# Kernel tuning notes

Hardware: AMD Instinct MI355X
Metric: run time of the kernel (lower is better)

The kernel has to match this reference:

```python
import jax, jax.numpy as jnp
import numpy as np

B, N, H = 8192, 8, 1024  # batch, DOF, hidden width; state dim = 2*N


def setup_inputs() -> dict:
    key = jax.random.key(0)
    ks = jax.random.split(key, 4)
    s1 = 1.0 / np.sqrt(2 * N)
    s2 = 1.0 / np.sqrt(H)
    return {
        "x": jax.random.normal(ks[0], (B, 2 * N), dtype=jnp.float32),
        "W1": jax.random.normal(ks[1], (2 * N, H), dtype=jnp.float32) * s1,
        "b1": jnp.zeros((H,), dtype=jnp.float32),
        "W2": jax.random.normal(ks[2], (H, H), dtype=jnp.float32) * s2,
        "b2": jnp.zeros((H,), dtype=jnp.float32),
        "W3": jax.random.normal(ks[3], (H, 1), dtype=jnp.float32) * s2,
        "b3": jnp.zeros((1,), dtype=jnp.float32),
    }


def reference(x, W1, b1, W2, b2, W3, b3):
    def lagrangian(q, qd):
        z = jnp.concatenate([q, qd])           # (2N,)
        h = jax.nn.softplus(z @ W1 + b1)
        h = jax.nn.softplus(h @ W2 + b2)
        return (h @ W3 + b3).sum()             # scalar L(q, qd)

    dL_dq_fn = jax.grad(lagrangian, argnums=0)
    dL_dqd_fn = jax.grad(lagrangian, argnums=1)
    # forward-over-reverse Hessian blocks (cheap: only N tangents)
    H_qdqd_fn = jax.jacfwd(dL_dqd_fn, argnums=1)   # d2L/dqd dqd, (N,N)
    H_qddq_fn = jax.jacfwd(dL_dqd_fn, argnums=0)   # d2L/dqd dq,  (N,N)

    def step(xi):
        q, qd = xi[:N], xi[N:]
        dL_dq = dL_dq_fn(q, qd)                      # (N,)
        M = H_qdqd_fn(q, qd)                         # mass-matrix block
        C = H_qddq_fn(q, qd)
        qdd = jnp.linalg.inv(M) @ (dL_dq - C @ qd)   # (N,)
        return jnp.concatenate([qd, qdd])            # (2N,)

    return jax.vmap(step)(x)
```

## Files before the change

kernel.cpp:

```cpp
#include <hip/hip_runtime.h>
#include <math.h>

#define B_ 8192
#define H_ 1024
#define LDP0 136
#define LDT 148

#define A_SEC 145
#define B_SEC 129
#define A_GRN (12*A_SEC)
#define B_GRN (12*B_SEC)
#define AB_SH ((A_GRN + B_GRN)*8)

typedef short bfrag __attribute__((ext_vector_type(8)));
typedef float f4v  __attribute__((ext_vector_type(4)));

union U8 { unsigned short u[8]; uint4 v; };

__device__ __forceinline__ float sigf(float x){ return 1.0f/(1.0f+__expf(-x)); }

__device__ __forceinline__ unsigned int pkhi(unsigned int u1, unsigned int u0){
  return __builtin_amdgcn_perm(u1, u0, 0x07060302u);
}

__global__ void k1_s1(const float* __restrict__ x, const float* __restrict__ W1,
                      const float* __restrict__ b1, float* __restrict__ s1o){
  __shared__ float xs[16];
  int b = blockIdx.x, t = threadIdx.x;
  if(t < 16) xs[t] = x[b*16 + t];
  __syncthreads();
  for(int h = t; h < H_; h += 256){
    float acc = b1[h];
    #pragma unroll
    for(int j=0;j<16;j++) acc = __fmaf_rn(xs[j], W1[j*H_ + h], acc);
    s1o[(size_t)b*H_ + h] = sigf(acc);
  }
}

__global__ __launch_bounds__(256,3) void k2_s2(const float* __restrict__ s1,
                      const float* __restrict__ W2, const float* __restrict__ b2,
                      float* __restrict__ s2o){
  __shared__ __align__(16) float As[32*LDP0];
  __shared__ __align__(16) float Bs[32*LDP0];
  int t = threadIdx.x, tx = t & 15, ty = t >> 4;
  int m0 = blockIdx.x * 128, n0 = blockIdx.y * 128;
  int jj = t & 31, rb4 = (t >> 5) * 4;
  float acc[8][8];
  #pragma unroll
  for(int i=0;i<8;i++){
    #pragma unroll
    for(int k=0;k<8;k++) acc[i][k]=0.f; }

  for(int jt=0; jt<32; jt++){
    int j0 = jt*32;
    __syncthreads();
    #pragma unroll
    for(int g=0; g<4; g++){
      #pragma unroll
      for(int i=0;i<4;i++){
        int r = rb4 + i + 32*g;
        As[jj*LDP0 + r] = -__logf(1.0f - s1[(size_t)(m0+r)*H_ + j0 + jj]);
      }
    }
    { int jB = t >> 3, kb = (t & 7) * 16;
      const float* src = &W2[(size_t)(j0 + jB)*H_ + n0 + kb];
      #pragma unroll
      for(int c=0;c<4;c++) *(float4*)&Bs[jB*LDP0 + kb + 4*c] = *(const float4*)(src + 4*c);
    }
    __syncthreads();
    #pragma unroll 8
    for(int j=0;j<32;j++){
      float4 a0 = *(const float4*)&As[j*LDP0 + 8*ty];
      float4 a1f= *(const float4*)&As[j*LDP0 + 8*ty+4];
      float4 b0 = *(const float4*)&Bs[j*LDP0 + 4*tx];
      float4 b1f= *(const float4*)&Bs[j*LDP0 + 64 + 4*tx];
      float aa[8] = {a0.x,a0.y,a0.z,a0.w,a1f.x,a1f.y,a1f.z,a1f.w};
      float bb[8] = {b0.x,b0.y,b0.z,b0.w,b1f.x,b1f.y,b1f.z,b1f.w};
      #pragma unroll
      for(int i=0;i<8;i++){
        #pragma unroll
        for(int k=0;k<8;k++) acc[i][k] = __fmaf_rn(aa[i], bb[k], acc[i][k]); }
    }
  }
  float4 bb0 = *(const float4*)&b2[n0 + 4*tx];
  float4 bb1 = *(const float4*)&b2[n0 + 64 + 4*tx];
  #pragma unroll
  for(int i=0;i<8;i++){
    size_t r = (size_t)(m0 + 8*ty + i)*H_;
    float4 o0 = make_float4(sigf(acc[i][0]+bb0.x), sigf(acc[i][1]+bb0.y),
                            sigf(acc[i][2]+bb0.z), sigf(acc[i][3]+bb0.w));
    float4 o1 = make_float4(sigf(acc[i][4]+bb1.x), sigf(acc[i][5]+bb1.y),
                            sigf(acc[i][6]+bb1.z), sigf(acc[i][7]+bb1.w));
    *(float4*)&s2o[r + n0 + 4*tx] = o0;
    *(float4*)&s2o[r + n0 + 64 + 4*tx] = o1;
  }
}

__global__ __launch_bounds__(256,3) void k3_u(const float* __restrict__ s2,
                      const float* __restrict__ W2, const float* __restrict__ W3,
                      float* __restrict__ u){
  __shared__ __align__(16) float As[32*LDP0];
  __shared__ __align__(16) float Bs[32*LDP0];
  int t = threadIdx.x, tx = t & 15, ty = t >> 4;
  int m0 = blockIdx.x * 128, n0 = blockIdx.y * 128;
  int jj = t & 31, rb4 = (t >> 5) * 4;
  float acc[8][8];
  #pragma unroll
  for(int i=0;i<8;i++){
    #pragma unroll
    for(int k=0;k<8;k++) acc[i][k]=0.f; }

  for(int kt=0; kt<32; kt++){
    int k0 = kt*32;
    __syncthreads();
    float w3v = W3[k0 + jj];
    #pragma unroll
    for(int g=0; g<4; g++){
      #pragma unroll
      for(int i=0;i<4;i++){
        int r = rb4 + i + 32*g;
        As[jj*LDP0 + r] = w3v * s2[(size_t)(m0+r)*H_ + k0 + jj];
      }
    }
    { int jcol = t >> 1, kb = (t & 1) * 16;
      const float* src = &W2[(size_t)(n0 + jcol)*H_ + k0 + kb];
      #pragma unroll
      for(int c=0;c<16;c++) Bs[(kb+c)*LDP0 + jcol] = src[c];
    }
    __syncthreads();
    #pragma unroll 8
    for(int j=0;j<32;j++){
      float4 a0 = *(const float4*)&As[j*LDP0 + 8*ty];
      float4 a1f= *(const float4*)&As[j*LDP0 + 8*ty+4];
      float4 b0 = *(const float4*)&Bs[j*LDP0 + 4*tx];
      float4 b1f= *(const float4*)&Bs[j*LDP0 + 64 + 4*tx];
      float aa[8] = {a0.x,a0.y,a0.z,a0.w,a1f.x,a1f.y,a1f.z,a1f.w};
      float bb[8] = {b0.x,b0.y,b0.z,b0.w,b1f.x,b1f.y,b1f.z,b1f.w};
      #pragma unroll
      for(int i=0;i<8;i++){
        #pragma unroll
        for(int k=0;k<8;k++) acc[i][k] = __fmaf_rn(aa[i], bb[k], acc[i][k]); }
    }
  }
  #pragma unroll
  for(int i=0;i<8;i++){
    size_t r = (size_t)(m0 + 8*ty + i)*H_;
    *(float4*)&u[r + n0 + 4*tx]      = make_float4(acc[i][0],acc[i][1],acc[i][2],acc[i][3]);
    *(float4*)&u[r + n0 + 64 + 4*tx] = make_float4(acc[i][4],acc[i][5],acc[i][6],acc[i][7]);
  }
}

__global__ void kF(const float* __restrict__ W1, float* __restrict__ F64){
  int e = blockIdx.x*256 + threadIdx.x;
  int j = e >> 6, p = e & 63;
  F64[e] = W1[(8+(p>>3))*H_ + j] * W1[(8+(p&7))*H_ + j];
}

__global__ __launch_bounds__(256) void k5a(const float* __restrict__ s1,
                      const float* __restrict__ u, const float* __restrict__ F64,
                      float* __restrict__ Hz1M){
  __shared__ __align__(16) float As[32*72];
  __shared__ __align__(16) float Bs[32*72];
  int t = threadIdx.x, tx = t & 15, ty = t >> 4;
  int m0 = blockIdx.x * 64;
  int jj = t & 31, rb8 = (t >> 5) * 8;
  float acc[4][4];
  #pragma unroll
  for(int i=0;i<4;i++){
    #pragma unroll
    for(int k=0;k<4;k++) acc[i][k]=0.f; }

  for(int jt=0; jt<32; jt++){
    int j0 = jt*32;
    __syncthreads();
    #pragma unroll
    for(int g=0; g<8; g++){
      int r = rb8 + g;
      float s = s1[(size_t)(m0+r)*H_ + j0 + jj];
      As[jj*72 + r] = s*(1.0f-s)*u[(size_t)(m0+r)*H_ + j0 + jj];
    }
    { int jB = t >> 3, cb = (t & 7) * 8;
      const float* src = &F64[(j0 + jB)*64 + cb];
      *(float4*)&Bs[jB*72 + cb]   = *(const float4*)(src);
      *(float4*)&Bs[jB*72 + cb+4] = *(const float4*)(src+4);
    }
    __syncthreads();
    #pragma unroll 8
    for(int j=0;j<32;j++){
      float4 a4 = *(const float4*)&As[j*72 + 4*ty];
      float4 b4 = *(const float4*)&Bs[j*72 + 4*tx];
      float aa[4] = {a4.x,a4.y,a4.z,a4.w};
      float bb[4] = {b4.x,b4.y,b4.z,b4.w};
      #pragma unroll
      for(int i=0;i<4;i++){
        #pragma unroll
        for(int k=0;k<4;k++) acc[i][k] = __fmaf_rn(aa[i], bb[k], acc[i][k]); }
    }
  }
  #pragma unroll
  for(int i=0;i<4;i++)
    *(float4*)&Hz1M[(size_t)(m0+4*ty+i)*64 + 4*tx] =
      make_float4(acc[i][0],acc[i][1],acc[i][2],acc[i][3]);
}

__global__ void k5b(const float* __restrict__ s1, const float* __restrict__ u,
                    const float* __restrict__ W1, const float* __restrict__ x,
                    float* __restrict__ dq16){
  int wid = threadIdx.x >> 6, lane = threadIdx.x & 63;
  int b = blockIdx.x*4 + wid;
  float qd[8];
  #pragma unroll
  for(int i=0;i<8;i++) qd[i] = x[b*16 + 8 + i];
  float accd[8] = {0,0,0,0,0,0,0,0};
  float accc[8] = {0,0,0,0,0,0,0,0};
  for(int jb=0;jb<16;jb++){
    int j = jb*64 + lane;
    float s1v = s1[(size_t)b*H_+j], uv = u[(size_t)b*H_+j];
    float g1 = s1v*uv;
    float d1 = (1.0f - s1v)*g1;
    float w1q = 0.f;
    #pragma unroll
    for(int i=0;i<8;i++){ float w = W1[i*H_+j];
      accd[i] = __fmaf_rn(g1, w, accd[i]);
      w1q = __fmaf_rn(qd[i], w, w1q); }
    float dw = d1*w1q;
    #pragma unroll
    for(int m=0;m<8;m++) accc[m] = __fmaf_rn(dw, W1[(8+m)*H_+j], accc[m]);
  }
  #pragma unroll
  for(int i=0;i<8;i++){
    #pragma unroll
    for(int off=1; off<64; off<<=1){
      accd[i] += __shfl_xor(accd[i], off, 64);
      accc[i] += __shfl_xor(accc[i], off, 64);
    }
  }
  if(lane==0){
    #pragma unroll
    for(int i=0;i<8;i++){ dq16[b*16+i] = accd[i]; dq16[b*16+8+i] = accc[i]; }
  }
}

__global__ void kW2T(const float* __restrict__ W2, unsigned short* __restrict__ Wh,
                     unsigned short* __restrict__ Wm, unsigned short* __restrict__ Wl){
  __shared__ float tile[32][132];
  int j0 = blockIdx.x * 32, k0 = blockIdx.y * 128;
  int t = threadIdx.x;
  int lr = t >> 3, lc0 = (t & 7) * 16;
  const float* src = &W2[(size_t)(j0+lr)*H_ + k0 + lc0];
  #pragma unroll
  for(int c=0;c<16;c+=4) *(float4*)&tile[lr][lc0+c] = *(const float4*)(src + c);
  __syncthreads();
  int k = t >> 1;
  #pragma unroll
  for(int o2=0;o2<2;o2++){
    int oc = (t&1)*2 + o2;
    U8 uh, um2, ul2;
    #pragma unroll
    for(int e=0;e<8;e++){
      float a = tile[oc*8+e][k];
      unsigned int ua = __float_as_uint(a);
      unsigned int h = ua & 0xFFFF0000u;
      float r1 = __fsub_rn(a, __uint_as_float(h));
      unsigned int m = __float_as_uint(r1) & 0xFFFF0000u;
      float l = __fsub_rn(r1, __uint_as_float(m));
      uh.u[e]  = (unsigned short)(h >> 16);
      um2.u[e] = (unsigned short)(m >> 16);
      ul2.u[e] = (unsigned short)(__float_as_uint(l) >> 16);
    }
    size_t o = (size_t)(k0+k)*H_ + j0 + oc*8;
    *(uint4*)&Wh[o] = uh.v; *(uint4*)&Wm[o] = um2.v; *(uint4*)&Wl[o] = ul2.v;
  }
}

__global__ __launch_bounds__(256,3) void k4_mfma(
    const float* __restrict__ s1, const float* __restrict__ s2,
    const float* __restrict__ x,  const float* __restrict__ W1,
    const unsigned short* __restrict__ W2Th, const unsigned short* __restrict__ W2Tm,
    const unsigned short* __restrict__ W2Tl,
    const float* __restrict__ W3, float* __restrict__ Mpart){
  __shared__ union {
    unsigned short AB[AB_SH];
    float Td[64*LDT];
  } sm;
  __shared__ float qds[16][8];

  int t = threadIdx.x;
  int wv = t >> 6, lane = t & 63;
  int kb = blockIdx.x & 7, sgp = blockIdx.x >> 3;
  int b0 = sgp*16, k0 = kb*128;

  if(t < 128){ int s = t>>3, i = t&7; qds[s][i] = x[(b0+s)*16 + 8+i]; }

  f4v acc[9][2];
  #pragma unroll
  for(int mt=0;mt<9;mt++){
    #pragma unroll
    for(int n2=0;n2<2;n2++){ acc[mt][n2][0]=0.f; acc[mt][n2][1]=0.f; acc[mt][n2][2]=0.f; acc[mt][n2][3]=0.f; }
  }

  int aoct = t & 3, arow = t >> 2;
  int bn = t >> 1;
  int fr_m = lane & 15, fr_q = lane >> 4;
  int pfm   = fr_m ^ ((fr_m & 8) >> 1);
  int aRd   = fr_q*A_SEC + pfm;
  int bRd   = A_GRN + fr_q*B_SEC + (2*wv)*16 + pfm;
  int bPerm = A_GRN + (bn ^ ((bn & 8) >> 1));

  for(int jt=0; jt<32; jt++){
    int j0 = jt*32;
    __syncthreads();
    #pragma unroll
    for(int pass=0; pass<3; pass++){
      int r = pass*64 + arow;
      if(r < 144){
        float4 w0, w1v, sa, sb;
        if(r < 128){
          int s = r>>3, m = r&7;
          const float* wp = &W1[(size_t)(8+m)*H_ + j0 + aoct*8];
          w0 = *(const float4*)wp; w1v = *(const float4*)(wp+4);
          const float* sp = &s1[(size_t)(b0+s)*H_ + j0 + aoct*8];
          sa = *(const float4*)sp; sb = *(const float4*)(sp+4);
        } else {
          int s = r - 128;
          float g0=0,g1=0,g2=0,g3=0,g4=0,g5=0,g6=0,g7=0;
          #pragma unroll
          for(int i=0;i<8;i++){
            float q = qds[s][i];
            const float* wp = &W1[(size_t)i*H_ + j0 + aoct*8];
            float4 a0 = *(const float4*)wp, a1 = *(const float4*)(wp+4);
            g0 = __fmaf_rn(q, a0.x, g0); g1 = __fmaf_rn(q, a0.y, g1);
            g2 = __fmaf_rn(q, a0.z, g2); g3 = __fmaf_rn(q, a0.w, g3);
            g4 = __fmaf_rn(q, a1.x, g4); g5 = __fmaf_rn(q, a1.y, g5);
            g6 = __fmaf_rn(q, a1.z, g6); g7 = __fmaf_rn(q, a1.w, g7);
          }
          w0 = make_float4(g0,g1,g2,g3); w1v = make_float4(g4,g5,g6,g7);
          const float* sp = &s1[(size_t)(b0+s)*H_ + j0 + aoct*8];
          sa = *(const float4*)sp; sb = *(const float4*)(sp+4);
        }
        float av[8];
        av[0]=__fmul_rn(w0.x,sa.x); av[1]=__fmul_rn(w0.y,sa.y);
        av[2]=__fmul_rn(w0.z,sa.z); av[3]=__fmul_rn(w0.w,sa.w);
        av[4]=__fmul_rn(w1v.x,sb.x); av[5]=__fmul_rn(w1v.y,sb.y);
        av[6]=__fmul_rn(w1v.z,sb.z); av[7]=__fmul_rn(w1v.w,sb.w);
        unsigned int uh[8], um[8], ul[8];
        #pragma unroll
        for(int e=0;e<8;e++){
          unsigned int ua = __float_as_uint(av[e]);
          unsigned int h = ua & 0xFFFF0000u;
          float r1 = __fsub_rn(av[e], __uint_as_float(h));
          unsigned int m = __float_as_uint(r1) & 0xFFFF0000u;
          float l = __fsub_rn(r1, __uint_as_float(m));
          uh[e]=h; um[e]=m; ul[e]=__float_as_uint(l);
        }
        int g0i = aoct*A_SEC + (r ^ ((r & 8) >> 1));
        uint4 vh = make_uint4(pkhi(uh[1],uh[0]), pkhi(uh[3],uh[2]), pkhi(uh[5],uh[4]), pkhi(uh[7],uh[6]));
        uint4 vm = make_uint4(pkhi(um[1],um[0]), pkhi(um[3],um[2]), pkhi(um[5],um[4]), pkhi(um[7],um[6]));
        uint4 vl = make_uint4(pkhi(ul[1],ul[0]), pkhi(ul[3],ul[2]), pkhi(ul[5],ul[4]), pkhi(ul[7],ul[6]));
        *(uint4*)&sm.AB[(g0i            )*8] = vh;
        *(uint4*)&sm.AB[(g0i + 4*A_SEC  )*8] = vm;
        *(uint4*)&sm.AB[(g0i + 8*A_SEC  )*8] = vl;
      }
    }
    #pragma unroll
    for(int o2=0;o2<2;o2++){
      int oc = (t&1)*2 + o2;
      size_t gsrc = (size_t)(k0+bn)*H_ + j0 + oc*8;
      int g0i = bPerm + oc*B_SEC;
      *(uint4*)&sm.AB[(g0i            )*8] = *(const uint4*)&W2Th[gsrc];
      *(uint4*)&sm.AB[(g0i + 4*B_SEC  )*8] = *(const uint4*)&W2Tm[gsrc];
      *(uint4*)&sm.AB[(g0i + 8*B_SEC  )*8] = *(const uint4*)&W2Tl[gsrc];
    }
    __syncthreads();
    bfrag bf[2][3];
    #pragma unroll
    for(int n2=0;n2<2;n2++){
      #pragma unroll
      for(int p=0;p<3;p++) bf[n2][p] = *(bfrag*)&sm.AB[(bRd + p*4*B_SEC + n2*16)*8];
    }
    #pragma unroll
    for(int mt=0; mt<9; mt++){
      bfrag a0 = *(bfrag*)&sm.AB[(aRd             + mt*16)*8];
      bfrag a1v= *(bfrag*)&sm.AB[(aRd + 4*A_SEC   + mt*16)*8];
      bfrag a2v= *(bfrag*)&sm.AB[(aRd + 8*A_SEC   + mt*16)*8];
      #pragma unroll
      for(int n2=0;n2<2;n2++){
        f4v c = acc[mt][n2];
        c = __builtin_amdgcn_mfma_f32_16x16x32_bf16(a2v, bf[n2][1], c, 0,0,0);
        c = __builtin_amdgcn_mfma_f32_16x16x32_bf16(a1v, bf[n2][2], c, 0,0,0);
        c = __builtin_amdgcn_mfma_f32_16x16x32_bf16(a2v, bf[n2][0], c, 0,0,0);
        c = __builtin_amdgcn_mfma_f32_16x16x32_bf16(a0,  bf[n2][2], c, 0,0,0);
        c = __builtin_amdgcn_mfma_f32_16x16x32_bf16(a1v, bf[n2][1], c, 0,0,0);
        c = __builtin_amdgcn_mfma_f32_16x16x32_bf16(a1v, bf[n2][0], c, 0,0,0);
        c = __builtin_amdgcn_mfma_f32_16x16x32_bf16(a0,  bf[n2][1], c, 0,0,0);
        c = __builtin_amdgcn_mfma_f32_16x16x32_bf16(a0,  bf[n2][0], c, 0,0,0);
        acc[mt][n2] = c;
      }
    }
  }

  float Mp[44];
  #pragma unroll
  for(int i=0;i<44;i++) Mp[i]=0.f;
  int es = t>>4, ec = t&15;
  const float* s2p = &s2[(size_t)(b0+es)*H_ + k0];

  #pragma unroll
  for(int ph=0; ph<2; ph++){
    __syncthreads();
    if((wv>>1) == ph){
      int w1b = wv & 1;
      #pragma unroll
      for(int mt=0; mt<9; mt++){
        #pragma unroll
        for(int n2=0;n2<2;n2++){
          int col = (2*w1b+n2)*16 + fr_m;
          int rowb = mt*16 + fr_q*4;
          #pragma unroll
          for(int rg=0;rg<4;rg++)
            sm.Td[col*LDT + rowb + rg] = acc[mt][n2][rg];
        }
      }
    }
    __syncthreads();
    float4 s2v = *(const float4*)&s2p[ph*64 + ec*4];
    float4 w3v = *(const float4*)&W3[k0 + ph*64 + ec*4];
    float dv[4] = { w3v.x*s2v.x*(1.f-s2v.x), w3v.y*s2v.y*(1.f-s2v.y),
                    w3v.z*s2v.z*(1.f-s2v.z), w3v.w*s2v.w*(1.f-s2v.w) };
    #pragma unroll
    for(int e=0;e<4;e++){
      int col = ec*4+e;
      const float* tp = &sm.Td[col*LDT + es*8];
      float4 t0 = *(const float4*)tp, t1 = *(const float4*)(tp+4);
      float T8[8] = {t0.x,t0.y,t0.z,t0.w,t1.x,t1.y,t1.z,t1.w};
      float vv = sm.Td[col*LDT + 128 + es];
      float d = dv[e];
      int ix=0;
      #pragma unroll
      for(int m=0;m<8;m++){
        float w = __fmul_rn(T8[m], d);
        Mp[36+m] = __fmaf_rn(w, vv, Mp[36+m]);
        #pragma unroll
        for(int n=m;n<8;n++){ Mp[ix] = __fmaf_rn(w, T8[n], Mp[ix]); ix++; }
      }
    }
  }
  #pragma unroll
  for(int i=0;i<44;i++){
    #pragma unroll
    for(int off=1; off<16; off<<=1) Mp[i] += __shfl_xor(Mp[i], off, 64);
  }
  if(ec==0){
    float* o = &Mpart[((size_t)(b0+es)*8 + kb)*44];
    #pragma unroll
    for(int i=0;i<44;i++) o[i] = Mp[i];
  }
}

__global__ __launch_bounds__(64) void k6(const float* __restrict__ x,
                    const float* __restrict__ Hz1M, const float* __restrict__ Mpart,
                    const float* __restrict__ dq16, float* __restrict__ out){
  __shared__ double A[64][73];
  int t = threadIdx.x;
  int b = blockIdx.x*64 + t;
  double* Ar = A[t];
  float qd[8];
  #pragma unroll
  for(int j=0;j<8;j++) qd[j] = x[b*16 + 8 + j];
  double Ms[44];
  #pragma unroll
  for(int i=0;i<44;i++) Ms[i]=0.0;
  for(int kb=0;kb<8;kb++){
    const float* mp = &Mpart[((size_t)b*8+kb)*44];
    #pragma unroll
    for(int i=0;i<44;i++) Ms[i] += (double)mp[i];
  }
  #pragma unroll
  for(int i=0;i<8;i++){
    #pragma unroll
    for(int j=0;j<8;j++) Ar[i*9+j] = (double)Hz1M[(size_t)b*64 + i*8 + j];
    Ar[i*9+8] = (double)dq16[b*16+i] - (double)dq16[b*16+8+i] - Ms[36+i];
  }
  { int ix=0;
    for(int m=0;m<8;m++)
      for(int n=m;n<8;n++){
        Ar[m*9+n] += Ms[ix];
        if(n>m) Ar[n*9+m] += Ms[ix];
        ix++;
      }
  }
  for(int c=0;c<8;c++){
    int piv = c; double best = fabs(Ar[c*9+c]);
    for(int rr=c+1; rr<8; rr++){ double v = fabs(Ar[rr*9+c]); if(v>best){best=v;piv=rr;} }
    if(piv!=c){
      for(int cc=c; cc<9; cc++){ double tmp=Ar[c*9+cc]; Ar[c*9+cc]=Ar[piv*9+cc]; Ar[piv*9+cc]=tmp; }
    }
    double inv = 1.0/Ar[c*9+c];
    for(int rr=c+1; rr<8; rr++){
      double f = Ar[rr*9+c]*inv;
      for(int cc=c+1; cc<9; cc++) Ar[rr*9+cc] -= f*Ar[c*9+cc];
    }
  }
  double sol[8];
  #pragma unroll
  for(int i=7;i>=0;i--){
    double s = Ar[i*9+8];
    #pragma unroll
    for(int j=i+1;j<8;j++) s -= Ar[i*9+j]*sol[j];
    sol[i] = s/Ar[i*9+i];
  }
  #pragma unroll
  for(int j=0;j<8;j++) out[b*16+j] = qd[j];
  #pragma unroll
  for(int i=0;i<8;i++) out[b*16+8+i] = (float)sol[i];
}

extern "C" void kernel_launch(void* const* d_in, const int* in_sizes, int n_in,
                              void* d_out, int out_size, void* d_ws, size_t ws_size,
                              hipStream_t stream){
  const float* x  = (const float*)d_in[0];
  const float* W1 = (const float*)d_in[1];
  const float* b1 = (const float*)d_in[2];
  const float* W2 = (const float*)d_in[3];
  const float* b2 = (const float*)d_in[4];
  const float* W3 = (const float*)d_in[5];
  float* out = (float*)d_out;

  float* ws   = (float*)d_ws;
  size_t BH   = (size_t)B_*H_;
  float* s1   = ws;
  float* s2   = s1  + BH;
  float* u    = s2  + BH;
  float* F64  = u   + BH;
  float* Hz1M = F64 + (size_t)H_*64;
  float* dq16 = Hz1M+ (size_t)B_*64;

  float* Mpart = u;
  unsigned short* W2Th = (unsigned short*)(u + 3145728);
  unsigned short* W2Tm = W2Th + (size_t)H_*H_;
  unsigned short* W2Tl = W2Tm + (size_t)H_*H_;

  k1_s1 <<<dim3(B_),      dim3(256), 0, stream>>>(x, W1, b1, s1);
  k2_s2 <<<dim3(64,8),    dim3(256), 0, stream>>>(s1, W2, b2, s2);
  k3_u  <<<dim3(64,8),    dim3(256), 0, stream>>>(s2, W2, W3, u);
  kF    <<<dim3(256),     dim3(256), 0, stream>>>(W1, F64);
  k5a   <<<dim3(128),     dim3(256), 0, stream>>>(s1, u, F64, Hz1M);
  k5b   <<<dim3(2048),    dim3(256), 0, stream>>>(s1, u, W1, x, dq16);
  kW2T  <<<dim3(32,8),    dim3(256), 0, stream>>>(W2, W2Th, W2Tm, W2Tl);
  k4_mfma<<<dim3(4096),   dim3(256), 0, stream>>>(s1, s2, x, W1, W2Th, W2Tm, W2Tl, W3, Mpart);
  k6    <<<dim3(128),     dim3(64),  0, stream>>>(x, Hz1M, Mpart, dq16, out);
}
```

Baseline: 2.182 ms.

## Load W2 B-fragments directly from global into registers, drop LDS staging

Each wave now loads its own W2 bf16 hi/mid/lo fragments straight from global memory into registers at the top of each j-tile, and no longer stages them through shared memory. This shrinks the LDS footprint to the A operand only, and the occupancy hint rises from 3 to 4 blocks per CU. It removes the LDS store/load round trip for B. In exchange each wave issues uncoalesced 16-byte global loads per row, and register pressure rises under the tighter launch bound.

```diff
diff --git a/kernel.cpp b/kernel.cpp
--- a/kernel.cpp
+++ b/kernel.cpp
@@ -7,10 +7,7 @@
 #define LDT 148
 
 #define A_SEC 145
-#define B_SEC 129
 #define A_GRN (12*A_SEC)
-#define B_GRN (12*B_SEC)
-#define AB_SH ((A_GRN + B_GRN)*8)
 
 typedef short bfrag __attribute__((ext_vector_type(8)));
 typedef float f4v  __attribute__((ext_vector_type(4)));
@@ -273,14 +270,14 @@
   }
 }
 
-__global__ __launch_bounds__(256,3) void k4_mfma(
+__global__ __launch_bounds__(256,4) void k4_mfma(
     const float* __restrict__ s1, const float* __restrict__ s2,
     const float* __restrict__ x,  const float* __restrict__ W1,
     const unsigned short* __restrict__ W2Th, const unsigned short* __restrict__ W2Tm,
     const unsigned short* __restrict__ W2Tl,
     const float* __restrict__ W3, float* __restrict__ Mpart){
   __shared__ union {
-    unsigned short AB[AB_SH];
+    unsigned short A[A_GRN*8];
     float Td[64*LDT];
   } sm;
   __shared__ float qds[16][8];
@@ -300,15 +297,21 @@
   }
 
   int aoct = t & 3, arow = t >> 2;
-  int bn = t >> 1;
   int fr_m = lane & 15, fr_q = lane >> 4;
   int pfm   = fr_m ^ ((fr_m & 8) >> 1);
   int aRd   = fr_q*A_SEC + pfm;
-  int bRd   = A_GRN + fr_q*B_SEC + (2*wv)*16 + pfm;
-  int bPerm = A_GRN + (bn ^ ((bn & 8) >> 1));
 
   for(int jt=0; jt<32; jt++){
     int j0 = jt*32;
+    bfrag bf[2][3];
+    #pragma unroll
+    for(int n2=0;n2<2;n2++){
+      int n = (2*wv+n2)*16 + fr_m;
+      size_t gb = (size_t)(k0+n)*H_ + j0 + fr_q*8;
+      bf[n2][0] = *(const bfrag*)&W2Th[gb];
+      bf[n2][1] = *(const bfrag*)&W2Tm[gb];
+      bf[n2][2] = *(const bfrag*)&W2Tl[gb];
+    }
     __syncthreads();
     #pragma unroll
     for(int pass=0; pass<3; pass++){
@@ -357,32 +360,17 @@
         uint4 vh = make_uint4(pkhi(uh[1],uh[0]), pkhi(uh[3],uh[2]), pkhi(uh[5],uh[4]), pkhi(uh[7],uh[6]));
         uint4 vm = make_uint4(pkhi(um[1],um[0]), pkhi(um[3],um[2]), pkhi(um[5],um[4]), pkhi(um[7],um[6]));
         uint4 vl = make_uint4(pkhi(ul[1],ul[0]), pkhi(ul[3],ul[2]), pkhi(ul[5],ul[4]), pkhi(ul[7],ul[6]));
-        *(uint4*)&sm.AB[(g0i            )*8] = vh;
-        *(uint4*)&sm.AB[(g0i + 4*A_SEC  )*8] = vm;
-        *(uint4*)&sm.AB[(g0i + 8*A_SEC  )*8] = vl;
-      }
-    }
-    #pragma unroll
-    for(int o2=0;o2<2;o2++){
-      int oc = (t&1)*2 + o2;
-      size_t gsrc = (size_t)(k0+bn)*H_ + j0 + oc*8;
-      int g0i = bPerm + oc*B_SEC;
-      *(uint4*)&sm.AB[(g0i            )*8] = *(const uint4*)&W2Th[gsrc];
-      *(uint4*)&sm.AB[(g0i + 4*B_SEC  )*8] = *(const uint4*)&W2Tm[gsrc];
-      *(uint4*)&sm.AB[(g0i + 8*B_SEC  )*8] = *(const uint4*)&W2Tl[gsrc];
-    }
-    __syncthreads();
-    bfrag bf[2][3];
-    #pragma unroll
-    for(int n2=0;n2<2;n2++){
-      #pragma unroll
-      for(int p=0;p<3;p++) bf[n2][p] = *(bfrag*)&sm.AB[(bRd + p*4*B_SEC + n2*16)*8];
-    }
+        *(uint4*)&sm.A[(g0i            )*8] = vh;
+        *(uint4*)&sm.A[(g0i + 4*A_SEC  )*8] = vm;
+        *(uint4*)&sm.A[(g0i + 8*A_SEC  )*8] = vl;
+      }
+    }
+    __syncthreads();
     #pragma unroll
     for(int mt=0; mt<9; mt++){
-      bfrag a0 = *(bfrag*)&sm.AB[(aRd             + mt*16)*8];
-      bfrag a1v= *(bfrag*)&sm.AB[(aRd + 4*A_SEC   + mt*16)*8];
-      bfrag a2v= *(bfrag*)&sm.AB[(aRd + 8*A_SEC   + mt*16)*8];
+      bfrag a0 = *(bfrag*)&sm.A[(aRd             + mt*16)*8];
+      bfrag a1v= *(bfrag*)&sm.A[(aRd + 4*A_SEC   + mt*16)*8];
+      bfrag a2v= *(bfrag*)&sm.A[(aRd + 8*A_SEC   + mt*16)*8];
       #pragma unroll
       for(int n2=0;n2<2;n2++){
         f4v c = acc[mt][n2];
```

Measured after the change: 3.196 ms. +46.5%, slower.

## Double k4_mfma output tile width to halve A-tile rebuild work

Applied to the files above, without the earlier changes.

Each k4_mfma block now covers 256 output columns of the hidden layer instead of 128, so each wave computes four 16-column MFMA tiles rather than two. The grid shrinks from 4096 to 2048 blocks. The A tile, which is rebuilt per block with three-way bf16 splitting and tangent computation, is now reused across twice as many columns, cutting redundant A-side global loads and conversion work. The cost is twice as many accumulator registers, larger shared memory for the B tile, and occupancy lowered from 3 to 2 blocks per CU. The epilogue runs in four phases and writes the partial results in the same two 128-column chunks as before.

```diff
diff --git a/kernel.cpp b/kernel.cpp
--- a/kernel.cpp
+++ b/kernel.cpp
@@ -7,10 +7,10 @@
 #define LDT 148
 
 #define A_SEC 145
-#define B_SEC 129
+#define B2_SEC 257
 #define A_GRN (12*A_SEC)
-#define B_GRN (12*B_SEC)
-#define AB_SH ((A_GRN + B_GRN)*8)
+#define B2_GRN (12*B2_SEC)
+#define AB2_SH ((A_GRN + B2_GRN)*8)
 
 typedef short bfrag __attribute__((ext_vector_type(8)));
 typedef float f4v  __attribute__((ext_vector_type(4)));
@@ -273,30 +273,30 @@
   }
 }
 
-__global__ __launch_bounds__(256,3) void k4_mfma(
+__global__ __launch_bounds__(256,2) void k4_mfma(
     const float* __restrict__ s1, const float* __restrict__ s2,
     const float* __restrict__ x,  const float* __restrict__ W1,
     const unsigned short* __restrict__ W2Th, const unsigned short* __restrict__ W2Tm,
     const unsigned short* __restrict__ W2Tl,
     const float* __restrict__ W3, float* __restrict__ Mpart){
   __shared__ union {
-    unsigned short AB[AB_SH];
+    unsigned short AB[AB2_SH];
     float Td[64*LDT];
   } sm;
   __shared__ float qds[16][8];
 
   int t = threadIdx.x;
   int wv = t >> 6, lane = t & 63;
-  int kb = blockIdx.x & 7, sgp = blockIdx.x >> 3;
-  int b0 = sgp*16, k0 = kb*128;
+  int kb2 = blockIdx.x & 3, sgp = blockIdx.x >> 2;
+  int b0 = sgp*16, k0 = kb2*256;
 
   if(t < 128){ int s = t>>3, i = t&7; qds[s][i] = x[(b0+s)*16 + 8+i]; }
 
-  f4v acc[9][2];
+  f4v acc[9][4];
   #pragma unroll
   for(int mt=0;mt<9;mt++){
     #pragma unroll
-    for(int n2=0;n2<2;n2++){ acc[mt][n2][0]=0.f; acc[mt][n2][1]=0.f; acc[mt][n2][2]=0.f; acc[mt][n2][3]=0.f; }
+    for(int n2=0;n2<4;n2++){ acc[mt][n2][0]=0.f; acc[mt][n2][1]=0.f; acc[mt][n2][2]=0.f; acc[mt][n2][3]=0.f; }
   }
 
   int aoct = t & 3, arow = t >> 2;
@@ -304,8 +304,10 @@
   int fr_m = lane & 15, fr_q = lane >> 4;
   int pfm   = fr_m ^ ((fr_m & 8) >> 1);
   int aRd   = fr_q*A_SEC + pfm;
-  int bRd   = A_GRN + fr_q*B_SEC + (2*wv)*16 + pfm;
-  int bPerm = A_GRN + (bn ^ ((bn & 8) >> 1));
+  int bRd   = A_GRN + fr_q*B2_SEC + wv*64 + pfm;
+  int bW0   = A_GRN + (bn ^ ((bn & 8) >> 1));
+  int bn2   = bn + 128;
+  int bW1   = A_GRN + (bn2 ^ ((bn2 & 8) >> 1));
 
   for(int jt=0; jt<32; jt++){
     int j0 = jt*32;
@@ -365,18 +367,23 @@
     #pragma unroll
     for(int o2=0;o2<2;o2++){
       int oc = (t&1)*2 + o2;
-      size_t gsrc = (size_t)(k0+bn)*H_ + j0 + oc*8;
-      int g0i = bPerm + oc*B_SEC;
-      *(uint4*)&sm.AB[(g0i            )*8] = *(const uint4*)&W2Th[gsrc];
-      *(uint4*)&sm.AB[(g0i + 4*B_SEC  )*8] = *(const uint4*)&W2Tm[gsrc];
-      *(uint4*)&sm.AB[(g0i + 8*B_SEC  )*8] = *(const uint4*)&W2Tl[gsrc];
-    }
-    __syncthreads();
-    bfrag bf[2][3];
-    #pragma unroll
-    for(int n2=0;n2<2;n2++){
-      #pragma unroll
-      for(int p=0;p<3;p++) bf[n2][p] = *(bfrag*)&sm.AB[(bRd + p*4*B_SEC + n2*16)*8];
+      size_t gs0 = (size_t)(k0+bn )*H_ + j0 + oc*8;
+      size_t gs1 = (size_t)(k0+bn2)*H_ + j0 + oc*8;
+      int w0i = bW0 + oc*B2_SEC;
+      int w1i = bW1 + oc*B2_SEC;
+      *(uint4*)&sm.AB[(w0i             )*8] = *(const uint4*)&W2Th[gs0];
+      *(uint4*)&sm.AB[(w0i + 4*B2_SEC  )*8] = *(const uint4*)&W2Tm[gs0];
+      *(uint4*)&sm.AB[(w0i + 8*B2_SEC  )*8] = *(const uint4*)&W2Tl[gs0];
+      *(uint4*)&sm.AB[(w1i             )*8] = *(const uint4*)&W2Th[gs1];
+      *(uint4*)&sm.AB[(w1i + 4*B2_SEC  )*8] = *(const uint4*)&W2Tm[gs1];
+      *(uint4*)&sm.AB[(w1i + 8*B2_SEC  )*8] = *(const uint4*)&W2Tl[gs1];
+    }
+    __syncthreads();
+    bfrag bf[4][3];
+    #pragma unroll
+    for(int n2=0;n2<4;n2++){
+      #pragma unroll
+      for(int p=0;p<3;p++) bf[n2][p] = *(bfrag*)&sm.AB[(bRd + p*4*B2_SEC + n2*16)*8];
     }
     #pragma unroll
     for(int mt=0; mt<9; mt++){
@@ -384,7 +391,7 @@
       bfrag a1v= *(bfrag*)&sm.AB[(aRd + 4*A_SEC   + mt*16)*8];
       bfrag a2v= *(bfrag*)&sm.AB[(aRd + 8*A_SEC   + mt*16)*8];
       #pragma unroll
-      for(int n2=0;n2<2;n2++){
+      for(int n2=0;n2<4;n2++){
         f4v c = acc[mt][n2];
         c = __builtin_amdgcn_mfma_f32_16x16x32_bf16(a2v, bf[n2][1], c, 0,0,0);
         c = __builtin_amdgcn_mfma_f32_16x16x32_bf16(a1v, bf[n2][2], c, 0,0,0);
@@ -406,15 +413,14 @@
   const float* s2p = &s2[(size_t)(b0+es)*H_ + k0];
 
   #pragma unroll
-  for(int ph=0; ph<2; ph++){
-    __syncthreads();
-    if((wv>>1) == ph){
-      int w1b = wv & 1;
+  for(int ph=0; ph<4; ph++){
+    __syncthreads();
+    if(wv == ph){
       #pragma unroll
       for(int mt=0; mt<9; mt++){
         #pragma unroll
-        for(int n2=0;n2<2;n2++){
-          int col = (2*w1b+n2)*16 + fr_m;
+        for(int n2=0;n2<4;n2++){
+          int col = n2*16 + fr_m;
           int rowb = mt*16 + fr_q*4;
           #pragma unroll
           for(int rg=0;rg<4;rg++)
@@ -444,16 +450,21 @@
         for(int n=m;n<8;n++){ Mp[ix] = __fmaf_rn(w, T8[n], Mp[ix]); ix++; }
       }
     }
-  }
-  #pragma unroll
-  for(int i=0;i<44;i++){
-    #pragma unroll
-    for(int off=1; off<16; off<<=1) Mp[i] += __shfl_xor(Mp[i], off, 64);
-  }
-  if(ec==0){
-    float* o = &Mpart[((size_t)(b0+es)*8 + kb)*44];
-    #pragma unroll
-    for(int i=0;i<44;i++) o[i] = Mp[i];
+    if(ph & 1){
+      #pragma unroll
+      for(int i=0;i<44;i++){
+        #pragma unroll
+        for(int off=1; off<16; off<<=1) Mp[i] += __shfl_xor(Mp[i], off, 64);
+      }
+      if(ec==0){
+        int kb = kb2*2 + (ph>>1);
+        float* o = &Mpart[((size_t)(b0+es)*8 + kb)*44];
+        #pragma unroll
+        for(int i=0;i<44;i++) o[i] = Mp[i];
+      }
+      #pragma unroll
+      for(int i=0;i<44;i++) Mp[i]=0.f;
+    }
   }
 }
 
@@ -547,6 +558,6 @@
   k5a   <<<dim3(128),     dim3(256), 0, stream>>>(s1, u, F64, Hz1M);
   k5b   <<<dim3(2048),    dim3(256), 0, stream>>>(s1, u, W1, x, dq16);
   kW2T  <<<dim3(32,8),    dim3(256), 0, stream>>>(W2, W2Th, W2Tm, W2Tl);
-  k4_mfma<<<dim3(4096),   dim3(256), 0, stream>>>(s1, s2, x, W1, W2Th, W2Tm, W2Tl, W3, Mpart);
+  k4_mfma<<<dim3(2048),   dim3(256), 0, stream>>>(s1, s2, x, W1, W2Th, W2Tm, W2Tl, W3, Mpart);
   k6    <<<dim3(128),     dim3(64),  0, stream>>>(x, Hz1M, Mpart, dq16, out);
 }
```

Result: faster. 1.998 ms (-8.4%).
